# Kernel tuning notes

Measured on AMD Instinct MI355X. Metric: run time of the kernel, lower is better.

## Reference

```python
import jax, jax.numpy as jnp
import numpy as np

SCORE_THRESHOLD = 0.5
NMS_TOP_K = 1024
NMS_THRESHOLD = 0.6
N_ANCHORS = 262144
N_CLASSES = 80


def setup_inputs() -> dict:
    key = jax.random.key(0)
    k1, k2, k3 = jax.random.split(key, 3)
    # valid xyxy boxes: x1<x2, y1<y2
    xy = jax.random.uniform(k1, (1, N_ANCHORS, 2), minval=0.0, maxval=2048.0)
    wh = jax.random.uniform(k2, (1, N_ANCHORS, 2), minval=1.0, maxval=64.0)
    pred_bboxes = jnp.concatenate([xy, xy + wh], axis=-1)  # [1, N, 4]
    pred_scores = jax.random.uniform(k3, (1, N_ANCHORS, N_CLASSES))  # [1, N, C]
    return {"pred_bboxes": pred_bboxes, "pred_scores": pred_scores}


def _pairwise_iou(boxes):
    # boxes: [K, 4] xyxy -> [K, K] IoU
    area = (boxes[:, 2] - boxes[:, 0]) * (boxes[:, 3] - boxes[:, 1])
    lt = jnp.maximum(boxes[:, None, :2], boxes[None, :, :2])
    rb = jnp.minimum(boxes[:, None, 2:], boxes[None, :, 2:])
    wh = jnp.clip(rb - lt, 0.0)
    inter = wh[..., 0] * wh[..., 1]
    union = area[:, None] + area[None, :] - inter
    return inter / jnp.maximum(union, 1e-9)


def reference(pred_bboxes, pred_scores):
    scores = pred_scores[0]  # [N, C]
    boxes = pred_bboxes[0]   # [N, 4]

    # single-label-per-box branch: per-anchor best class
    conf = jnp.max(scores, axis=1)      # [N]
    label = jnp.argmax(scores, axis=1)  # [N] int

    # score threshold (masking instead of data-dependent filtering)
    masked_conf = jnp.where(conf >= SCORE_THRESHOLD, conf, -1.0)

    # top-k candidates (sorted descending, matching torch.topk)
    top_conf, top_idx = jax.lax.top_k(masked_conf, NMS_TOP_K)  # [K]
    top_boxes = boxes[top_idx]   # [K, 4]
    top_label = label[top_idx]   # [K]
    valid = top_conf >= SCORE_THRESHOLD  # [K] rows that passed the threshold

    # batched_nms trick: offset boxes per class so cross-class IoU is ~0
    max_coord = jax.lax.stop_gradient(jnp.max(top_boxes)) + 1.0
    offset_boxes = top_boxes + top_label.astype(top_boxes.dtype)[:, None] * max_coord
    iou = _pairwise_iou(offset_boxes)  # [K, K]

    # sequential greedy suppression in score order (rows already sorted)
    idx = jnp.arange(NMS_TOP_K)

    def body(i, keep):
        suppress = (iou[i] > NMS_THRESHOLD) & (idx > i) & keep[i] & keep
        return keep & ~suppress

    keep = jax.lax.fori_loop(0, NMS_TOP_K, body, valid)  # [K] bool

    out = jnp.concatenate(
        [top_boxes, top_conf[:, None], top_label.astype(top_boxes.dtype)[:, None]],
        axis=1,
    )  # [K, 6] = [x1, y1, x2, y2, conf, label]
    # fixed-shape masked output: suppressed / invalid rows zeroed
    return out * keep[:, None].astype(out.dtype)
```

## Files before the change

kernel.cpp:

```cpp
#include <hip/hip_runtime.h>
#include <stdint.h>


#define N_ANCH   262144
#define N_CLS    80
#define K_TOP    1024
#define CAP      4096

typedef unsigned long long ull;

#define HSLOT(b) ((((b) & 2047u) << 4) | ((b) >> 11))
#define SKEW(e) ((uint32_t)(e) + ((uint32_t)(e) >> 4))

#define OFF_HIST  0
#define OFF_CTRL  131072
#define MEMSET_BYTES 131136
#define OFF_BINS  131136
#define OFF_LIST  655424
#define WS_REQUIRED 688192

__global__ __launch_bounds__(256) void k_sentinel(float* __restrict__ out, float v) {
    int i = blockIdx.x * 256 + threadIdx.x;
    if (i < K_TOP * 6) out[i] = v;
}

static __device__ __forceinline__ uint32_t conf_key24(float best) {
    uint32_t u = __float_as_uint(best);
    if (u > 0x3F800000u) u = 0x3F800000u;
    if (u < 0x3F000000u) u = 0x3F000000u;
    return u - 0x3F000000u;
}

static __device__ __forceinline__ void cmpsw(ull& x, ull& y, bool up) {
    ull mn = x < y ? x : y, mx = x < y ? y : x;
    x = up ? mn : mx; y = up ? mx : mn;
}
static __device__ __forceinline__ void cmpswu(uint32_t& x, uint32_t& y, bool up) {
    uint32_t mn = x < y ? x : y, mx = x < y ? y : x;
    x = up ? mn : mx; y = up ? mx : mn;
}

__global__ __launch_bounds__(256) void k_conf(const float* __restrict__ scores,
                                              uint16_t* __restrict__ bins16,
                                              uint32_t* __restrict__ hist) {
    const int t = threadIdx.x;
    const int r = t >> 4, s = t & 15;
    const int a0 = blockIdx.x * 128 + r;
    const float* base = scores + (size_t)a0 * N_CLS;
    float4 v0 = ((const float4*)base)[s];
    float4 v1;
    if (s < 4) v1 = ((const float4*)base)[16 + s];
    #pragma unroll
    for (int i = 0; i < 8; i++) {
        float4 c0 = v0, c1 = v1;
        if (i + 1 < 8) {
            const float* nb = base + (size_t)(i + 1) * 16 * N_CLS;
            v0 = ((const float4*)nb)[s];
            if (s < 4) v1 = ((const float4*)nb)[16 + s];
        }
        float best = c0.x; int lab = 4 * s;
        if (c0.y > best) { best = c0.y; lab = 4 * s + 1; }
        if (c0.z > best) { best = c0.z; lab = 4 * s + 2; }
        if (c0.w > best) { best = c0.w; lab = 4 * s + 3; }
        if (s < 4) {
            const int c = 64 + 4 * s;
            if (c1.x > best) { best = c1.x; lab = c; }
            if (c1.y > best) { best = c1.y; lab = c + 1; }
            if (c1.z > best) { best = c1.z; lab = c + 2; }
            if (c1.w > best) { best = c1.w; lab = c + 3; }
        }
        ull key = ((ull)(uint32_t)__float_as_uint(best) << 7) | (ull)(uint32_t)(127 - lab);
        ull o;
        o = __shfl_xor(key, 1); if (o > key) key = o;
        o = __shfl_xor(key, 2); if (o > key) key = o;
        o = __shfl_xor(key, 4); if (o > key) key = o;
        o = __shfl_xor(key, 8); if (o > key) key = o;
        if (s == 0) {
            const int a = a0 + i * 16;
            float bv = __uint_as_float((uint32_t)(key >> 7));
            uint16_t pk = 0;
            if (bv >= 0.5f) {
                uint32_t bin = conf_key24(bv) >> 8;
                if (bin > 32767u) bin = 32767u;
                atomicAdd(&hist[HSLOT(bin)], 1u);
                pk = (uint16_t)(0x8000u | bin);
            }
            bins16[a] = pk;
        }
    }
}

__global__ __launch_bounds__(1024) void k_cut(const uint32_t* __restrict__ hist,
                                              uint32_t* __restrict__ ctrl) {
    __shared__ uint32_t wtot[16], wsuf[16];
    const int t = threadIdx.x;
    const int lane = t & 63, w = t >> 6;
    const uint32_t sbase = (((uint32_t)t & 63u) << 9) | ((uint32_t)t >> 6);
    uint32_t c[32];
    #pragma unroll
    for (int i = 0; i < 32; i++) c[i] = hist[sbase | ((uint32_t)i << 4)];
    uint32_t part = 0;
    #pragma unroll
    for (int i = 0; i < 32; i++) part += c[i];
    uint32_t x = part;
    #pragma unroll
    for (int d = 1; d < 64; d <<= 1) {
        uint32_t o = __shfl_down(x, d);
        if (lane + d < 64) x += o;
    }
    if (lane == 0) wtot[w] = x;
    __syncthreads();
    if (t < 16) {
        uint32_t s = 0;
        for (int ww = t + 1; ww < 16; ww++) s += wtot[ww];
        wsuf[t] = s;
        if (t == 0) {
            uint32_t total = s + wtot[0];
            ctrl[1] = (total < K_TOP) ? total : K_TOP;
        }
    }
    __syncthreads();
    uint32_t run = (x + wsuf[w]) - part;
    if (run < K_TOP && run + part >= K_TOP) {
        uint32_t fnd = 0, cbv = 0;
        #pragma unroll
        for (int i = 31; i >= 0; i--) {
            if (!fnd && run + c[i] >= K_TOP) { cbv = (uint32_t)(t * 32 + i); fnd = 1; }
            if (!fnd) run += c[i];
        }
        ctrl[2] = cbv;
    }
}

__global__ __launch_bounds__(256) void k_gather(const float* __restrict__ scores,
                                                const uint16_t* __restrict__ bins16,
                                                uint32_t* __restrict__ ctrl,
                                                ull* __restrict__ list) {
    __shared__ uint32_t lcnt, lbase;
    const int t = threadIdx.x, b = blockIdx.x;
    if (t == 0) { lcnt = 0; lbase = 0; }
    __syncthreads();
    const uint32_t cT = ctrl[2];
    const int a4 = b * 256 + t;
    ushort4 pk4 = ((const ushort4*)bins16)[a4];
    uint16_t pk[4] = {pk4.x, pk4.y, pk4.z, pk4.w};
    ull      hk[4];
    uint32_t hs[4];
    bool     hv[4];
    #pragma unroll
    for (int e = 0; e < 4; e++) {
        hv[e] = false; hk[e] = 0; hs[e] = 0;
        uint32_t u = pk[e];
        if ((u & 0x8000u) && (u & 0x7FFFu) >= cT) {
            const uint32_t a = (uint32_t)a4 * 4u + (uint32_t)e;
            const float4* row = (const float4*)(scores + (size_t)a * N_CLS);
            float best = -1.f; int lab = 0;
            for (int f = 0; f < 20; f++) {
                float4 w = row[f];
                if (w.x > best) { best = w.x; lab = 4 * f; }
                if (w.y > best) { best = w.y; lab = 4 * f + 1; }
                if (w.z > best) { best = w.z; lab = 4 * f + 2; }
                if (w.w > best) { best = w.w; lab = 4 * f + 3; }
            }
            if (best >= 0.5f) {
                uint32_t k24 = conf_key24(best);
                hk[e] = ((ull)(0x1000000u - k24) << 25) | ((ull)a << 7)
                      | (ull)(uint32_t)lab;
                hs[e] = atomicAdd(&lcnt, 1u);
                hv[e] = true;
            }
        }
    }
    __syncthreads();
    if (t == 0 && lcnt) lbase = atomicAdd(&ctrl[0], lcnt);
    __syncthreads();
    const uint32_t base2 = lbase;
    #pragma unroll
    for (int e = 0; e < 4; e++) {
        if (hv[e]) {
            uint32_t slot = base2 + hs[e];
            if (slot < CAP) list[slot] = hk[e];
        }
    }
}

__global__ __launch_bounds__(1024) void k_final(const float4* __restrict__ bboxes,
                                                const uint32_t* __restrict__ ctrl,
                                                const ull* __restrict__ list,
                                                float* __restrict__ out) {
    __shared__ __align__(16) char smem[34816];
    ull*      sk    = (ull*)smem;
    float4*   ob    = (float4*)smem;
    float*    ar    = (float*)(smem + 16384);
    float*    red16 = (float*)(smem + 20480);
    uint32_t* g     = (uint32_t*)(smem + 20544);
    ull*      sup   = (ull*)(smem + 24640);
    uint8_t*  keepA = (uint8_t*)(smem + 32832);
    uint32_t* cnt   = (uint32_t*)(smem + 33856);
    uint32_t* stt   = (uint32_t*)(smem + 34176);
    uint8_t*  ovr   = (uint8_t*)(smem + 34496);
    const int t = threadIdx.x;
    const uint32_t nsel = ctrl[1];
    uint32_t ncand = ctrl[0]; if (ncand > CAP) ncand = CAP;

    uint32_t nsort = 1024;
    while (nsort < ncand) nsort <<= 1;
    const int TS = (int)(nsort >> 2);
    ull E[4];
    if (t < TS) {
        #pragma unroll
        for (int rr = 0; rr < 4; rr++) {
            int e = 4 * t + rr;
            E[rr] = (e < (int)ncand) ? list[e] : ~0ull;
        }
    }
    for (uint32_t k = 2; k <= nsort; k <<= 1) {
        for (uint32_t j = k >> 1; j > 0; j >>= 1) {
            if (j >= 256) {
                __syncthreads();
                if (t < TS) {
                    #pragma unroll
                    for (int rr = 0; rr < 4; rr++) sk[SKEW(4 * t + rr)] = E[rr];
                }
                __syncthreads();
                if (t < TS) {
                    #pragma unroll
                    for (int rr = 0; rr < 4; rr++) {
                        uint32_t e = 4 * t + rr;
                        ull o = sk[SKEW(e ^ j)];
                        bool keepMax = (((e & k) == 0) != ((e & j) == 0));
                        bool gt = E[rr] > o;
                        E[rr] = (gt == keepMax) ? E[rr] : o;
                    }
                }
            } else if (t < TS) {
                if (j >= 4) {
                    int d = (int)(j >> 2);
                    #pragma unroll
                    for (int rr = 0; rr < 4; rr++) {
                        uint32_t e = 4 * t + rr;
                        ull o = __shfl_xor(E[rr], d);
                        bool keepMax = (((e & k) == 0) != ((e & j) == 0));
                        bool gt = E[rr] > o;
                        E[rr] = (gt == keepMax) ? E[rr] : o;
                    }
                } else if (j == 2) {
                    bool up = (((4 * t) & k) == 0);
                    cmpsw(E[0], E[2], up); cmpsw(E[1], E[3], up);
                } else {
                    bool upA = (((4 * t) & k) == 0);
                    bool upB = (((4 * t + 2) & k) == 0);
                    cmpsw(E[0], E[1], upA);
                    cmpsw(E[2], E[3], upB);
                }
            }
        }
    }
    __syncthreads();
    if (t < TS) {
        #pragma unroll
        for (int rr = 0; rr < 4; rr++) sk[SKEW(4 * t + rr)] = E[rr];
    }
    __syncthreads();
    ull skey = sk[SKEW(t)];
    __syncthreads();

    float4 bx = make_float4(0.f, 0.f, 0.f, 0.f);
    float cf = 0.f, lb = 0.f;
    uint32_t lab = 0;
    if ((uint32_t)t < nsel) {
        uint32_t idx = (uint32_t)(skey >> 7) & 0x3FFFFu;
        lab = (uint32_t)skey & 127u;
        cf = __uint_as_float(0x3F000000u + (0x1000000u - (uint32_t)(skey >> 25)));
        lb = (float)lab;
        bx = bboxes[idx];
    }
    float m = fmaxf(fmaxf(bx.x, bx.y), fmaxf(bx.z, bx.w));
    for (int d = 32; d > 0; d >>= 1) m = fmaxf(m, __shfl_xor(m, d));
    if ((t & 63) == 0) red16[t >> 6] = m;
    __syncthreads();
    float M = red16[0];
    #pragma unroll
    for (int w = 1; w < 16; w++) M = fmaxf(M, red16[w]);
    M = __fadd_rn(M, 1.0f);
    float o = __fmul_rn(lb, M);
    float4 q;
    q.x = __fadd_rn(bx.x, o); q.y = __fadd_rn(bx.y, o);
    q.z = __fadd_rn(bx.z, o); q.w = __fadd_rn(bx.w, o);
    ob[t] = q;
    ar[t] = __fmul_rn(__fsub_rn(q.z, q.x), __fsub_rn(q.w, q.y));
    g[t] = ((uint32_t)t < nsel) ? ((lab << 10) | (uint32_t)t) : 0xFFFFFFFFu;
    if (t < N_CLS) { cnt[t] = 0; ovr[t] = 0; stt[t] = 0; }
    keepA[t] = 0;
    __syncthreads();

    uint32_t G[4];
    if (t < 256) {
        #pragma unroll
        for (int rr = 0; rr < 4; rr++) G[rr] = g[4 * t + rr];
    }
    for (int k = 2; k <= 1024; k <<= 1) {
        for (int j = k >> 1; j > 0; j >>= 1) {
            if (j >= 256) {
                __syncthreads();
                if (t < 256) {
                    #pragma unroll
                    for (int rr = 0; rr < 4; rr++) g[4 * t + rr] = G[rr];
                }
                __syncthreads();
                if (t < 256) {
                    #pragma unroll
                    for (int rr = 0; rr < 4; rr++) {
                        int e = 4 * t + rr;
                        uint32_t o2 = g[e ^ j];
                        bool keepMax = (((e & k) == 0) != ((e & j) == 0));
                        bool gt = G[rr] > o2;
                        G[rr] = (gt == keepMax) ? G[rr] : o2;
                    }
                }
            } else if (t < 256) {
                if (j >= 4) {
                    int d = j >> 2;
                    #pragma unroll
                    for (int rr = 0; rr < 4; rr++) {
                        int e = 4 * t + rr;
                        uint32_t o2 = (uint32_t)__shfl_xor((int)G[rr], d);
                        bool keepMax = (((e & k) == 0) != ((e & j) == 0));
                        bool gt = G[rr] > o2;
                        G[rr] = (gt == keepMax) ? G[rr] : o2;
                    }
                } else if (j == 2) {
                    bool up = (((4 * t) & k) == 0);
                    cmpswu(G[0], G[2], up); cmpswu(G[1], G[3], up);
                } else {
                    bool upA = (((4 * t) & k) == 0);
                    bool upB = (((4 * t + 2) & k) == 0);
                    cmpswu(G[0], G[1], upA); cmpswu(G[2], G[3], upB);
                }
            }
        }
    }
    __syncthreads();
    if (t < 256) {
        #pragma unroll
        for (int rr = 0; rr < 4; rr++) g[4 * t + rr] = G[rr];
    }
    __syncthreads();

    uint32_t gp = g[t];
    if (gp != 0xFFFFFFFFu) {
        uint32_t labp = gp >> 10;
        atomicAdd(&cnt[labp], 1u);
        if (t == 0 || (g[t - 1] >> 10) != labp) stt[labp] = (uint32_t)t;
    }
    __syncthreads();

    {
        ull sp = 0;
        if (gp != 0xFFFFFFFFu) {
            uint32_t labi = gp >> 10;
            uint32_t ri = gp & 1023u;
            float4 oi = ob[ri]; float ai = ar[ri];
            for (int qq = t + 1; qq < 1024; qq++) {
                uint32_t gq = g[qq];
                if ((gq >> 10) != labi) break;
                int dq = qq - t;
                if (dq > 64) { ovr[labi] = 1; break; }
                uint32_t rj = gq & 1023u;
                float4 oj = ob[rj];
                float lx = fmaxf(oi.x, oj.x), ly = fmaxf(oi.y, oj.y);
                float rx = fminf(oi.z, oj.z), ry = fminf(oi.w, oj.w);
                float wx = fmaxf(__fsub_rn(rx, lx), 0.f);
                float wy = fmaxf(__fsub_rn(ry, ly), 0.f);
                float inter = __fmul_rn(wx, wy);
                float uni = __fsub_rn(__fadd_rn(ai, ar[rj]), inter);
                float iou = __fdiv_rn(inter, fmaxf(uni, 1e-9f));
                if (iou > 0.6f) sp |= 1ull << (dq - 1);
            }
        }
        sup[t] = sp;
    }
    __syncthreads();

    if (t < N_CLS) {
        uint32_t n = cnt[t];
        if (n > 0) {
            uint32_t s0 = stt[t];
            if (n <= 64 && !ovr[t]) {
                ull kill = 0;
                for (uint32_t i = 0; i < n; i++) {
                    if (!((kill >> i) & 1ull)) {
                        if (i + 1 < 64) kill |= sup[s0 + i] << (i + 1);
                        keepA[g[s0 + i] & 1023u] = 1;
                    }
                }
            } else {
                for (uint32_t i = 0; i < n; i++) {
                    uint32_t ri = g[s0 + i] & 1023u;
                    float4 oi = ob[ri]; float ai = ar[ri];
                    bool kp = true;
                    for (uint32_t m2 = 0; m2 < i && kp; m2++) {
                        uint32_t rm = g[s0 + m2] & 1023u;
                        if (!keepA[rm]) continue;
                        float4 om = ob[rm];
                        float lx = fmaxf(om.x, oi.x), ly = fmaxf(om.y, oi.y);
                        float rx = fminf(om.z, oi.z), ry = fminf(om.w, oi.w);
                        float wx = fmaxf(__fsub_rn(rx, lx), 0.f);
                        float wy = fmaxf(__fsub_rn(ry, ly), 0.f);
                        float inter = __fmul_rn(wx, wy);
                        float uni = __fsub_rn(__fadd_rn(ar[rm], ai), inter);
                        float iou = __fdiv_rn(inter, fmaxf(uni, 1e-9f));
                        if (iou > 0.6f) kp = false;
                    }
                    keepA[ri] = kp ? 1 : 0;
                }
            }
        }
    }
    __syncthreads();

    const bool keep = keepA[t] != 0;
    float v0 = keep ? bx.x : 0.f, v1 = keep ? bx.y : 0.f;
    float v2 = keep ? bx.z : 0.f, v3 = keep ? bx.w : 0.f;
    float v4 = keep ? cf : 0.f, v5 = keep ? lb : 0.f;
    float2* o2 = (float2*)out;
    o2[t * 3 + 0] = make_float2(v0, v1);
    o2[t * 3 + 1] = make_float2(v2, v3);
    o2[t * 3 + 2] = make_float2(v4, v5);
}

extern "C" void kernel_launch(void* const* d_in, const int* in_sizes, int n_in,
                              void* d_out, int out_size, void* d_ws, size_t ws_size,
                              hipStream_t stream) {
    const float* bboxes = (const float*)d_in[0];
    const float* scores = (const float*)d_in[1];
    if (n_in >= 2 && in_sizes[0] > in_sizes[1]) {
        bboxes = (const float*)d_in[1];
        scores = (const float*)d_in[0];
    }

    if (ws_size < (size_t)WS_REQUIRED) {
        k_sentinel<<<(K_TOP * 6 + 255) / 256, 256, 0, stream>>>(
            (float*)d_out, (float)(ws_size >> 10));
        return;
    }

    char* ws = (char*)d_ws;
    uint32_t* hist   = (uint32_t*)(ws + OFF_HIST);
    uint32_t* ctrl   = (uint32_t*)(ws + OFF_CTRL);
    uint16_t* bins16 = (uint16_t*)(ws + OFF_BINS);
    ull*      list   = (ull*)(ws + OFF_LIST);

    hipMemsetAsync(ws, 0, MEMSET_BYTES, stream);
    k_conf  <<<N_ANCH / 128, 256, 0, stream>>>(scores, bins16, hist);
    k_cut   <<<1,           1024, 0, stream>>>(hist, ctrl);
    k_gather<<<256,          256, 0, stream>>>(scores, bins16, ctrl, list);
    k_final <<<1,           1024, 0, stream>>>((const float4*)bboxes, ctrl, list,
                                               (float*)d_out);
}
```

Baseline: 199.0 us.

## Replace class-grouping bitonic sort with bitmask counting sort; 2-per-thread candidate sort

In the final kernel, the 1024-element bitonic sort that groups candidates by class is replaced by a counting sort. Per-class membership bitmasks are built with shared atomicOr, then popcount gives class counts, prefix offsets and stable ranks. For candidate counts up to 2048, the main top-k sort now uses a 2-elements-per-thread bitonic layout with vectorised LDS exchanges instead of 4 per thread. This removes many sync-heavy sort stages at the cost of extra shared memory (45 KB) and a serial 80-step prefix loop.

```diff
diff --git a/kernel.cpp b/kernel.cpp
--- a/kernel.cpp
+++ b/kernel.cpp
@@ -33,10 +33,6 @@
 
 static __device__ __forceinline__ void cmpsw(ull& x, ull& y, bool up) {
     ull mn = x < y ? x : y, mx = x < y ? y : x;
-    x = up ? mn : mx; y = up ? mx : mn;
-}
-static __device__ __forceinline__ void cmpswu(uint32_t& x, uint32_t& y, bool up) {
-    uint32_t mn = x < y ? x : y, mx = x < y ? y : x;
     x = up ? mn : mx; y = up ? mx : mn;
 }
 
@@ -188,7 +184,7 @@
                                                 const uint32_t* __restrict__ ctrl,
                                                 const ull* __restrict__ list,
                                                 float* __restrict__ out) {
-    __shared__ __align__(16) char smem[34816];
+    __shared__ __align__(16) char smem[45056];
     ull*      sk    = (ull*)smem;
     float4*   ob    = (float4*)smem;
     float*    ar    = (float*)(smem + 16384);
@@ -199,70 +195,118 @@
     uint32_t* cnt   = (uint32_t*)(smem + 33856);
     uint32_t* stt   = (uint32_t*)(smem + 34176);
     uint8_t*  ovr   = (uint8_t*)(smem + 34496);
+    ull*      cmask = (ull*)(smem + 34816);
     const int t = threadIdx.x;
     const uint32_t nsel = ctrl[1];
     uint32_t ncand = ctrl[0]; if (ncand > CAP) ncand = CAP;
 
     uint32_t nsort = 1024;
     while (nsort < ncand) nsort <<= 1;
-    const int TS = (int)(nsort >> 2);
-    ull E[4];
-    if (t < TS) {
-        #pragma unroll
-        for (int rr = 0; rr < 4; rr++) {
-            int e = 4 * t + rr;
-            E[rr] = (e < (int)ncand) ? list[e] : ~0ull;
-        }
-    }
-    for (uint32_t k = 2; k <= nsort; k <<= 1) {
-        for (uint32_t j = k >> 1; j > 0; j >>= 1) {
-            if (j >= 256) {
-                __syncthreads();
-                if (t < TS) {
-                    #pragma unroll
-                    for (int rr = 0; rr < 4; rr++) sk[SKEW(4 * t + rr)] = E[rr];
+
+    if (nsort <= 2048) {
+        const int TS2 = (int)(nsort >> 1);
+        ull E0 = ~0ull, E1 = ~0ull;
+        if (t < TS2) {
+            int e = 2 * t;
+            E0 = (e < (int)ncand)     ? list[e]     : ~0ull;
+            E1 = (e + 1 < (int)ncand) ? list[e + 1] : ~0ull;
+        }
+        for (uint32_t k = 2; k <= nsort; k <<= 1) {
+            for (uint32_t j = k >> 1; j > 0; j >>= 1) {
+                if (j >= 128) {
+                    __syncthreads();
+                    if (t < TS2) {
+                        ulonglong2 wv; wv.x = E0; wv.y = E1;
+                        *(ulonglong2*)&sk[2 * t] = wv;
+                    }
+                    __syncthreads();
+                    if (t < TS2) {
+                        uint32_t e0 = 2 * t;
+                        ulonglong2 rv = *(const ulonglong2*)&sk[e0 ^ j];
+                        bool km = (((e0 & k) == 0) != ((e0 & j) == 0));
+                        E0 = ((E0 > rv.x) == km) ? E0 : rv.x;
+                        E1 = ((E1 > rv.y) == km) ? E1 : rv.y;
+                    }
+                } else if (t < TS2) {
+                    if (j >= 2) {
+                        int d = (int)(j >> 1);
+                        bool km = ((((2 * t) & k) == 0) != (((2 * t) & j) == 0));
+                        ull o0 = __shfl_xor(E0, d);
+                        ull o1 = __shfl_xor(E1, d);
+                        E0 = ((E0 > o0) == km) ? E0 : o0;
+                        E1 = ((E1 > o1) == km) ? E1 : o1;
+                    } else {
+                        bool up = (((2 * t) & k) == 0);
+                        cmpsw(E0, E1, up);
+                    }
                 }
-                __syncthreads();
-                if (t < TS) {
-                    #pragma unroll
-                    for (int rr = 0; rr < 4; rr++) {
-                        uint32_t e = 4 * t + rr;
-                        ull o = sk[SKEW(e ^ j)];
-                        bool keepMax = (((e & k) == 0) != ((e & j) == 0));
-                        bool gt = E[rr] > o;
-                        E[rr] = (gt == keepMax) ? E[rr] : o;
+            }
+        }
+        __syncthreads();
+        if (t < TS2) {
+            ulonglong2 wv; wv.x = E0; wv.y = E1;
+            *(ulonglong2*)&sk[2 * t] = wv;
+        }
+    } else {
+        const int TS = (int)(nsort >> 2);
+        ull E[4];
+        if (t < TS) {
+            #pragma unroll
+            for (int rr = 0; rr < 4; rr++) {
+                int e = 4 * t + rr;
+                E[rr] = (e < (int)ncand) ? list[e] : ~0ull;
+            }
+        }
+        for (uint32_t k = 2; k <= nsort; k <<= 1) {
+            for (uint32_t j = k >> 1; j > 0; j >>= 1) {
+                if (j >= 256) {
+                    __syncthreads();
+                    if (t < TS) {
+                        #pragma unroll
+                        for (int rr = 0; rr < 4; rr++) sk[SKEW(4 * t + rr)] = E[rr];
+                    }
+                    __syncthreads();
+                    if (t < TS) {
+                        #pragma unroll
+                        for (int rr = 0; rr < 4; rr++) {
+                            uint32_t e = 4 * t + rr;
+                            ull o = sk[SKEW(e ^ j)];
+                            bool keepMax = (((e & k) == 0) != ((e & j) == 0));
+                            bool gt = E[rr] > o;
+                            E[rr] = (gt == keepMax) ? E[rr] : o;
+                        }
+                    }
+                } else if (t < TS) {
+                    if (j >= 4) {
+                        int d = (int)(j >> 2);
+                        #pragma unroll
+                        for (int rr = 0; rr < 4; rr++) {
+                            uint32_t e = 4 * t + rr;
+                            ull o = __shfl_xor(E[rr], d);
+                            bool keepMax = (((e & k) == 0) != ((e & j) == 0));
+                            bool gt = E[rr] > o;
+                            E[rr] = (gt == keepMax) ? E[rr] : o;
+                        }
+                    } else if (j == 2) {
+                        bool up = (((4 * t) & k) == 0);
+                        cmpsw(E[0], E[2], up); cmpsw(E[1], E[3], up);
+                    } else {
+                        bool upA = (((4 * t) & k) == 0);
+                        bool upB = (((4 * t + 2) & k) == 0);
+                        cmpsw(E[0], E[1], upA);
+                        cmpsw(E[2], E[3], upB);
                     }
                 }
-            } else if (t < TS) {
-                if (j >= 4) {
-                    int d = (int)(j >> 2);
-                    #pragma unroll
-                    for (int rr = 0; rr < 4; rr++) {
-                        uint32_t e = 4 * t + rr;
-                        ull o = __shfl_xor(E[rr], d);
-                        bool keepMax = (((e & k) == 0) != ((e & j) == 0));
-                        bool gt = E[rr] > o;
-                        E[rr] = (gt == keepMax) ? E[rr] : o;
-                    }
-                } else if (j == 2) {
-                    bool up = (((4 * t) & k) == 0);
-                    cmpsw(E[0], E[2], up); cmpsw(E[1], E[3], up);
-                } else {
-                    bool upA = (((4 * t) & k) == 0);
-                    bool upB = (((4 * t + 2) & k) == 0);
-                    cmpsw(E[0], E[1], upA);
-                    cmpsw(E[2], E[3], upB);
-                }
-            }
-        }
-    }
-    __syncthreads();
-    if (t < TS) {
-        #pragma unroll
-        for (int rr = 0; rr < 4; rr++) sk[SKEW(4 * t + rr)] = E[rr];
-    }
-    __syncthreads();
-    ull skey = sk[SKEW(t)];
+            }
+        }
+        __syncthreads();
+        if (t < TS) {
+            #pragma unroll
+            for (int rr = 0; rr < 4; rr++) sk[SKEW(4 * t + rr)] = E[rr];
+        }
+    }
+    __syncthreads();
+    ull skey = (nsort <= 2048) ? sk[t] : sk[SKEW(t)];
     __syncthreads();
 
     float4 bx = make_float4(0.f, 0.f, 0.f, 0.f);
@@ -289,72 +333,44 @@
     q.z = __fadd_rn(bx.z, o); q.w = __fadd_rn(bx.w, o);
     ob[t] = q;
     ar[t] = __fmul_rn(__fsub_rn(q.z, q.x), __fsub_rn(q.w, q.y));
-    g[t] = ((uint32_t)t < nsel) ? ((lab << 10) | (uint32_t)t) : 0xFFFFFFFFu;
-    if (t < N_CLS) { cnt[t] = 0; ovr[t] = 0; stt[t] = 0; }
+    g[t] = 0xFFFFFFFFu;
+    if (t < N_CLS) ovr[t] = 0;
     keepA[t] = 0;
-    __syncthreads();
-
-    uint32_t G[4];
-    if (t < 256) {
+    if (t < 640) {
+        ulonglong2 z; z.x = 0; z.y = 0;
+        *(ulonglong2*)&cmask[2 * t] = z;
+    }
+    __syncthreads();
+
+    if ((uint32_t)t < nsel)
+        atomicOr(&cmask[lab * 16 + (t >> 6)], 1ull << (t & 63));
+    __syncthreads();
+    if (t < N_CLS) {
+        uint32_t s = 0;
         #pragma unroll
-        for (int rr = 0; rr < 4; rr++) G[rr] = g[4 * t + rr];
-    }
-    for (int k = 2; k <= 1024; k <<= 1) {
-        for (int j = k >> 1; j > 0; j >>= 1) {
-            if (j >= 256) {
-                __syncthreads();
-                if (t < 256) {
-                    #pragma unroll
-                    for (int rr = 0; rr < 4; rr++) g[4 * t + rr] = G[rr];
-                }
-                __syncthreads();
-                if (t < 256) {
-                    #pragma unroll
-                    for (int rr = 0; rr < 4; rr++) {
-                        int e = 4 * t + rr;
-                        uint32_t o2 = g[e ^ j];
-                        bool keepMax = (((e & k) == 0) != ((e & j) == 0));
-                        bool gt = G[rr] > o2;
-                        G[rr] = (gt == keepMax) ? G[rr] : o2;
-                    }
-                }
-            } else if (t < 256) {
-                if (j >= 4) {
-                    int d = j >> 2;
-                    #pragma unroll
-                    for (int rr = 0; rr < 4; rr++) {
-                        int e = 4 * t + rr;
-                        uint32_t o2 = (uint32_t)__shfl_xor((int)G[rr], d);
-                        bool keepMax = (((e & k) == 0) != ((e & j) == 0));
-                        bool gt = G[rr] > o2;
-                        G[rr] = (gt == keepMax) ? G[rr] : o2;
-                    }
-                } else if (j == 2) {
-                    bool up = (((4 * t) & k) == 0);
-                    cmpswu(G[0], G[2], up); cmpswu(G[1], G[3], up);
-                } else {
-                    bool upA = (((4 * t) & k) == 0);
-                    bool upB = (((4 * t + 2) & k) == 0);
-                    cmpswu(G[0], G[1], upA); cmpswu(G[2], G[3], upB);
-                }
-            }
-        }
-    }
-    __syncthreads();
-    if (t < 256) {
-        #pragma unroll
-        for (int rr = 0; rr < 4; rr++) g[4 * t + rr] = G[rr];
+        for (int w = 0; w < 16; w++) s += (uint32_t)__popcll(cmask[t * 16 + w]);
+        cnt[t] = s;
+    }
+    __syncthreads();
+    if (t < N_CLS) {
+        uint32_t s = 0;
+        for (int i = 0; i < N_CLS - 1; i++) {
+            uint32_t v = cnt[i];
+            if (i < t) s += v;
+        }
+        stt[t] = s;
+    }
+    __syncthreads();
+    if ((uint32_t)t < nsel) {
+        const ull* cm = &cmask[lab * 16];
+        uint32_t w = (uint32_t)t >> 6;
+        uint32_t r = (uint32_t)__popcll(cm[w] & ((1ull << (t & 63)) - 1ull));
+        for (uint32_t ww = 0; ww < w; ww++) r += (uint32_t)__popcll(cm[ww]);
+        g[stt[lab] + r] = (lab << 10) | (uint32_t)t;
     }
     __syncthreads();
 
     uint32_t gp = g[t];
-    if (gp != 0xFFFFFFFFu) {
-        uint32_t labp = gp >> 10;
-        atomicAdd(&cnt[labp], 1u);
-        if (t == 0 || (g[t - 1] >> 10) != labp) stt[labp] = (uint32_t)t;
-    }
-    __syncthreads();
-
     {
         ull sp = 0;
         if (gp != 0xFFFFFFFFu) {
```

Measured after the change: 187.1 us. -6.0%, faster.
